# Optimization experiments

Measured on AMD Instinct MI355X. Metric: run time of the kernel, lower is better.

## Reference

```python
import jax, jax.numpy as jnp
import numpy as np

M, N = 65536, 2048
VOL = (256.0, 256.0, 256.0)
EPS_QUAT = 1e-8
EPS_COV = 1e-6


def setup_inputs() -> dict:
    key = jax.random.key(0)
    k0, k1, k2, k3 = jax.random.split(key, 4)
    vol = jnp.asarray(VOL, dtype=jnp.float32)
    points = jax.random.uniform(k0, (M, 3), dtype=jnp.float32) * vol
    positions = jax.random.uniform(k1, (N, 3), dtype=jnp.float32) * vol
    initial_scale = min(VOL) / (N ** (1.0 / 3.0)) * 0.5
    log_scales = jnp.full((N, 3), np.float32(np.log(initial_scale)), dtype=jnp.float32)
    # near-identity quaternions (w ~ 1, small xyz) so rotation path is non-trivial
    rotations = jnp.concatenate(
        [jnp.ones((N, 1), jnp.float32), 0.1 * jax.random.normal(k2, (N, 3), jnp.float32)],
        axis=1,
    )
    weights = jax.random.uniform(k3, (N,), dtype=jnp.float32) * 0.1
    return {
        "points": points,
        "positions": positions,
        "log_scales": log_scales,
        "rotations": rotations,
        "weights": weights,
    }


def _quat_to_rot(q):
    # q: (N,4) normalized quaternions (w,x,y,z) -> (N,3,3)
    w, x, y, z = q[:, 0], q[:, 1], q[:, 2], q[:, 3]
    r00 = 1 - 2 * (y * y + z * z)
    r01 = 2 * (x * y - z * w)
    r02 = 2 * (x * z + y * w)
    r10 = 2 * (x * y + z * w)
    r11 = 1 - 2 * (x * x + z * z)
    r12 = 2 * (y * z - x * w)
    r20 = 2 * (x * z - y * w)
    r21 = 2 * (y * z + x * w)
    r22 = 1 - 2 * (x * x + y * y)
    R = jnp.stack(
        [jnp.stack([r00, r01, r02], -1),
         jnp.stack([r10, r11, r12], -1),
         jnp.stack([r20, r21, r22], -1)], axis=1)
    return R


def reference(points, positions, log_scales, rotations, weights):
    m, n = points.shape[0], positions.shape[0]
    scales = jnp.exp(log_scales)                                   # (N,3)
    quats = rotations / (jnp.linalg.norm(rotations, axis=1, keepdims=True) + EPS_QUAT)
    R = _quat_to_rot(quats)                                        # (N,3,3)
    # Sigma = R diag(s^2) R^T
    cov = jnp.einsum("nij,nj,nkj->nik", R, scales * scales, R)     # (N,3,3)
    A = jnp.linalg.inv(cov + EPS_COV * jnp.eye(3, dtype=cov.dtype))  # Sigma^{-1}, (N,3,3)
    # quad[m,n] = (p-u)^T A (p-u) = p^T A p - 2 p^T (A u) + u^T A u
    PP = (points[:, :, None] * points[:, None, :]).reshape(m, 9)   # (M,9)
    term_pp = PP @ A.reshape(n, 9).T                               # (M,N)
    b = jnp.einsum("nij,nj->ni", A, positions)                     # (N,3)
    term_pu = points @ b.T                                         # (M,N)
    term_uu = jnp.einsum("ni,ni->n", positions, b)                 # (N,)
    quad = term_pp - 2.0 * term_pu + term_uu[None, :]              # (M,N)
    g = jnp.exp(-0.5 * quad)                                       # (M,N)
    return g @ weights                                             # (M,)
```

## Files before the change

kernel.cpp:

```cpp
#include <hip/hip_runtime.h>
#include <math.h>

#define SCc     8
#define NSC     512
#define SCW     32.0f
#define NMAX    2048
#define GSLAB   2048
#define PSLAB   256
#define EVB     128
#define ECH     2
#define ELL     128
#define NSB     64
#define QCUT    22.0f

typedef float v2f __attribute__((ext_vector_type(2)));
static __device__ __forceinline__ v2f s2(float s) { v2f r; r.x = s; r.y = s; return r; }
static __device__ __forceinline__ v2f pkfma(v2f a, v2f b, v2f c) {
    return __builtin_elementwise_fma(a, b, c);
}
static __device__ __forceinline__ float fexp2(float x) {
#if __has_builtin(__builtin_amdgcn_exp2f)
    return __builtin_amdgcn_exp2f(x);
#else
    return exp2f(x);
#endif
}

static __device__ __forceinline__ int scell_of(float x, float y, float z) {
    int cx = min(SCc - 1, max(0, (int)(x * (1.0f / SCW))));
    int cy = min(SCc - 1, max(0, (int)(y * (1.0f / SCW))));
    int cz = min(SCc - 1, max(0, (int)(z * (1.0f / SCW))));
    return (cz << 6) | (cy << 3) | cx;
}

static __device__ __forceinline__ float cell_d2(int c, float mx, float my, float mz) {
    float lx = (c & 7) * SCW,        hx = lx + SCW;
    float ly = ((c >> 3) & 7) * SCW, hy = ly + SCW;
    float lz = (c >> 6) * SCW,       hz = lz + SCW;
    float dx = fmaxf(fmaxf(lx - mx, mx - hx), 0.0f);
    float dy = fmaxf(fmaxf(ly - my, my - hy), 0.0f);
    float dz = fmaxf(fmaxf(lz - mz, mz - hz), 0.0f);
    return dx * dx + dy * dy + dz * dz;
}

__global__ __launch_bounds__(256) void k_build(
    const float* __restrict__ positions,
    const float* __restrict__ log_scales,
    const float* __restrict__ rotations,
    const float* __restrict__ weights,
    float* __restrict__ params,
    unsigned* __restrict__ lcnt,
    unsigned* __restrict__ glists,
    unsigned* __restrict__ cnt,
    int N, int nPre)
{
    __shared__ float4 shaux[NMAX];
    __shared__ unsigned wc[4];
    int b   = (int)blockIdx.x;
    int tid = threadIdx.x;

    if (b < nPre) {
        int i = b * 256 + tid;
        if (i >= N) return;

        float s0 = expf(log_scales[3*i+0]);
        float s1 = expf(log_scales[3*i+1]);
        float s2_ = expf(log_scales[3*i+2]);
        float v0 = s0*s0, v1 = s1*s1, v2 = s2_*s2_;

        float qw = rotations[4*i+0], qx = rotations[4*i+1];
        float qy = rotations[4*i+2], qz = rotations[4*i+3];
        float inv = 1.0f / (sqrtf(qw*qw + qx*qx + qy*qy + qz*qz) + 1e-8f);
        qw *= inv; qx *= inv; qy *= inv; qz *= inv;

        float r00 = 1.f - 2.f*(qy*qy + qz*qz);
        float r01 = 2.f*(qx*qy - qz*qw);
        float r02 = 2.f*(qx*qz + qy*qw);
        float r10 = 2.f*(qx*qy + qz*qw);
        float r11 = 1.f - 2.f*(qx*qx + qz*qz);
        float r12 = 2.f*(qy*qz - qx*qw);
        float r20 = 2.f*(qx*qz - qy*qw);
        float r21 = 2.f*(qy*qz + qx*qw);
        float r22 = 1.f - 2.f*(qx*qx + qy*qy);

        float a = r00*r00*v0 + r01*r01*v1 + r02*r02*v2 + 1e-6f;
        float b_= r00*r10*v0 + r01*r11*v1 + r02*r12*v2;
        float c = r00*r20*v0 + r01*r21*v1 + r02*r22*v2;
        float d = r10*r10*v0 + r11*r11*v1 + r12*r12*v2 + 1e-6f;
        float e = r10*r20*v0 + r11*r21*v1 + r12*r22*v2;
        float f = r20*r20*v0 + r21*r21*v1 + r22*r22*v2 + 1e-6f;

        float m00 = d*f - e*e;
        float m01 = c*e - b_*f;
        float m02 = b_*e - c*d;
        float det = a*m00 + b_*m01 + c*m02;
        float id  = 1.0f / det;
        float A00 = m00*id, A01 = m01*id, A02 = m02*id;
        float A11 = (a*f - c*c)*id;
        float A12 = (c*b_ - a*e)*id;
        float A22 = (a*d - b_*b_)*id;

        float ux = positions[3*i+0], uy = positions[3*i+1], uz = positions[3*i+2];
        float bx = A00*ux + A01*uy + A02*uz;
        float by = A01*ux + A11*uy + A12*uz;
        float bz = A02*ux + A12*uy + A22*uz;
        float cq = ux*bx + uy*by + uz*bz;

        const float kk = -0.72134752044448170368f;
        float* P = params + 12*i;
        P[0]  = kk*A00;      P[1]  = kk*A11;      P[2]  = kk*A22;      P[3] = 2.f*kk*A01;
        P[4]  = 2.f*kk*A02;  P[5]  = 2.f*kk*A12;  P[6]  = -2.f*kk*bx;  P[7] = -2.f*kk*by;
        P[8]  = -2.f*kk*bz;  P[9]  = kk*cq;       P[10] = weights[i];  P[11] = 0.f;
        return;
    }
    if (b == nPre + NSC) {
        cnt[tid] = 0u; cnt[tid + 256] = 0u;
        return;
    }

    int c = b - nPre;
    const float L2E2 = 2.8853900817779268f;
    for (int g = tid; g < N; g += 256) {
        float v0 = fexp2(L2E2 * log_scales[3*g+0]);
        float v1 = fexp2(L2E2 * log_scales[3*g+1]);
        float v2 = fexp2(L2E2 * log_scales[3*g+2]);
        float lam = fmaxf(fmaxf(v0, v1), v2) + 1e-6f;
        float4 a;
        a.x = positions[3*g+0]; a.y = positions[3*g+1]; a.z = positions[3*g+2];
        a.w = QCUT * lam;
        shaux[g] = a;
    }
    __syncthreads();

    int lane = tid & 63;
    int w    = tid >> 6;
    unsigned long long lt = (1ULL << lane) - 1ULL;
    int Nq    = (N + 3) >> 2;
    int g0    = w * Nq;
    int g1    = min(N, g0 + Nq);
    int iters = (Nq + 63) >> 6;

    unsigned cw = 0;
    for (int it = 0; it < iters; ++it) {
        int g = g0 + it*64 + lane;
        bool keep = false;
        if (g < g1) { float4 a = shaux[g]; keep = cell_d2(c, a.x, a.y, a.z) <= a.w; }
        cw += (unsigned)__popcll(__ballot(keep));
    }
    if (lane == 0) wc[w] = cw;
    __syncthreads();
    unsigned pos = 0;
#pragma unroll
    for (int i = 0; i < 4; ++i) pos += (i < w) ? wc[i] : 0u;
    unsigned total = wc[0] + wc[1] + wc[2] + wc[3];
    unsigned* slab = glists + (size_t)c * GSLAB;
    for (int it = 0; it < iters; ++it) {
        int g = g0 + it*64 + lane;
        bool keep = false;
        if (g < g1) { float4 a = shaux[g]; keep = cell_d2(c, a.x, a.y, a.z) <= a.w; }
        unsigned long long mask = __ballot(keep);
        if (keep) {
            unsigned idx = pos + (unsigned)__popcll(mask & lt);
            if (idx < GSLAB) slab[idx] = (unsigned)g;
        }
        pos += (unsigned)__popcll(mask);
    }
    if (tid == 0) lcnt[c] = min(total, (unsigned)GSLAB);
}

__global__ __launch_bounds__(256) void k_scatter(
    const float* __restrict__ points, unsigned* __restrict__ cnt,
    float4* __restrict__ slabPts, int M)
{
    __shared__ unsigned lcur[NSC];
    __shared__ unsigned lbase[NSC];
    int tid = threadIdx.x;
    for (int i = tid; i < NSC; i += 256) lcur[i] = 0u;
    __syncthreads();
    int mh = (M + NSB - 1) / NSB;
    int m0 = (int)blockIdx.x * mh, m1 = min(M, m0 + mh);
    for (int m = m0 + tid; m < m1; m += 256) {
        int c = scell_of(points[3*m+0], points[3*m+1], points[3*m+2]);
        atomicAdd(&lcur[c], 1u);
    }
    __syncthreads();
    for (int i = tid; i < NSC; i += 256) {
        unsigned v = lcur[i];
        lbase[i] = v ? atomicAdd(&cnt[i], v) : 0u;
    }
    __syncthreads();
    for (int i = tid; i < NSC; i += 256) lcur[i] = 0u;
    __syncthreads();
    for (int m = m0 + tid; m < m1; m += 256) {
        float x = points[3*m+0], y = points[3*m+1], z = points[3*m+2];
        int c = scell_of(x, y, z);
        unsigned r = lbase[c] + atomicAdd(&lcur[c], 1u);
        if (r < PSLAB) {
            float4 sp; sp.x = x; sp.y = y; sp.z = z; sp.w = __uint_as_float((unsigned)m);
            slabPts[(size_t)c * PSLAB + r] = sp;
        }
    }
}

__global__ __launch_bounds__(EVB) void k_eval(
    const float4* __restrict__ slabPts, const float4* __restrict__ P4,
    const unsigned* __restrict__ cnt,  const unsigned* __restrict__ lcnt,
    const unsigned* __restrict__ glists,
    float* __restrict__ out)
{
    __shared__ float4 sl[ELL * 3];
    int c    = blockIdx.x;
    int tid  = threadIdx.x;
    int npts = min((int)cnt[c], PSLAB);
    int pb   = (int)blockIdx.y * EVB;
    if (pb >= npts) return;
    int pi   = pb + tid;
    bool act = pi < npts;

    float4 p = slabPts[(size_t)c * PSLAB + (act ? pi : 0)];
    float x = p.x, yv = p.y, zv = p.z;
    float xx = x*x, yy = yv*yv, zz = zv*zv;
    float xy = x*yv, xz = x*zv, yz = yv*zv;
    float acc = 0.f;

    int len = (int)lcnt[c];
    const unsigned* lst = glists + (size_t)c * GSLAB;

    for (int k0 = 0; k0 < len; k0 += ELL) {
        int kn = min(ELL, len - k0);
        __syncthreads();
        for (int e = tid; e < kn; e += EVB) {
            int g = (int)lst[k0 + e];
            sl[3*e + 0] = P4[3*g + 0];
            sl[3*e + 1] = P4[3*g + 1];
            sl[3*e + 2] = P4[3*g + 2];
        }
        __syncthreads();
#pragma unroll 2
        for (int e = 0; e < kn; ++e) {
            float4 q0 = sl[3*e + 0];
            float4 q1 = sl[3*e + 1];
            float4 q2 = sl[3*e + 2];

            float t0 = fmaf(q0.x, xx, q2.y);
            t0 = fmaf(q0.w, xy, t0);
            t0 = fmaf(q1.z, x,  t0);
            float t1 = q0.y * yy;
            t1 = fmaf(q1.y, yz, t1);
            t1 = fmaf(q1.w, yv, t1);
            float t2 = q0.z * zz;
            t2 = fmaf(q1.x, xz, t2);
            t2 = fmaf(q2.x, zv, t2);
            float e2 = (t0 + t1) + t2;
            acc = fmaf(q2.z, fexp2(e2), acc);
        }
    }
    if (act) out[__float_as_uint(p.w)] = acc;
}

#define NSPLIT 32
#define COARSEN 4
__global__ __launch_bounds__(256, 8) void gbf_eval_dense(
    const float* __restrict__ points,
    const float4* __restrict__ params,
    float* __restrict__ out, int M, int N, int nPer)
{
    int p0 = blockIdx.x * (256 * COARSEN) + threadIdx.x;
    int p1 = p0 + 256, p2 = p0 + 512, p3 = p0 + 768;
    int c0 = min(p0, M-1), c1 = min(p1, M-1), c2 = min(p2, M-1), c3 = min(p3, M-1);

    v2f X1, Y1, Z1, X2_, Y2_, Z2_;
    X1.x = points[3*c0+0]; X1.y = points[3*c1+0];
    Y1.x = points[3*c0+1]; Y1.y = points[3*c1+1];
    Z1.x = points[3*c0+2]; Z1.y = points[3*c1+2];
    X2_.x = points[3*c2+0]; X2_.y = points[3*c3+0];
    Y2_.x = points[3*c2+1]; Y2_.y = points[3*c3+1];
    Z2_.x = points[3*c2+2]; Z2_.y = points[3*c3+2];

    v2f XX1 = X1*X1, YY1 = Y1*Y1, ZZ1 = Z1*Z1;
    v2f XY1 = X1*Y1, XZ1 = X1*Z1, YZ1 = Y1*Z1;
    v2f XX2 = X2_*X2_, YY2 = Y2_*Y2_, ZZ2 = Z2_*Z2_;
    v2f XY2 = X2_*Y2_, XZ2 = X2_*Z2_, YZ2 = Y2_*Z2_;

    int jbase = blockIdx.y * nPer;
    int jend = min(nPer, N - jbase);
    int base = jbase * 3;
    v2f acc1; acc1.x = 0.f; acc1.y = 0.f;
    v2f acc2 = acc1;

#pragma unroll 2
    for (int j = 0; j < jend; ++j) {
        float4 q0 = params[base + 3*j + 0];
        float4 q1 = params[base + 3*j + 1];
        float4 q2 = params[base + 3*j + 2];
        v2f t0 = pkfma(s2(q0.x), XX1, s2(q2.y));
        t0 = pkfma(s2(q0.w), XY1, t0);
        t0 = pkfma(s2(q1.z), X1,  t0);
        v2f t1 = s2(q0.y) * YY1;
        t1 = pkfma(s2(q1.y), YZ1, t1);
        t1 = pkfma(s2(q1.w), Y1,  t1);
        v2f t2 = s2(q0.z) * ZZ1;
        t2 = pkfma(s2(q1.x), XZ1, t2);
        t2 = pkfma(s2(q2.x), Z1,  t2);
        v2f e1 = (t0 + t1) + t2;
        v2f u0 = pkfma(s2(q0.x), XX2, s2(q2.y));
        u0 = pkfma(s2(q0.w), XY2, u0);
        u0 = pkfma(s2(q1.z), X2_, u0);
        v2f u1 = s2(q0.y) * YY2;
        u1 = pkfma(s2(q1.y), YZ2, u1);
        u1 = pkfma(s2(q1.w), Y2_, u1);
        v2f u2 = s2(q0.z) * ZZ2;
        u2 = pkfma(s2(q1.x), XZ2, u2);
        u2 = pkfma(s2(q2.x), Z2_, u2);
        v2f e2 = (u0 + u1) + u2;
        v2f g1, g2;
        g1.x = fexp2(e1.x); g1.y = fexp2(e1.y);
        g2.x = fexp2(e2.x); g2.y = fexp2(e2.y);
        acc1 = pkfma(s2(q2.z), g1, acc1);
        acc2 = pkfma(s2(q2.z), g2, acc2);
    }
    if (p0 < M) atomicAdd(&out[p0], acc1.x);
    if (p1 < M) atomicAdd(&out[p1], acc1.y);
    if (p2 < M) atomicAdd(&out[p2], acc2.x);
    if (p3 < M) atomicAdd(&out[p3], acc2.y);
}

extern "C" void kernel_launch(void* const* d_in, const int* in_sizes, int n_in,
                              void* d_out, int out_size, void* d_ws, size_t ws_size,
                              hipStream_t stream)
{
    const float* points     = (const float*)d_in[0];
    const float* positions  = (const float*)d_in[1];
    const float* log_scales = (const float*)d_in[2];
    const float* rotations  = (const float*)d_in[3];
    const float* weights    = (const float*)d_in[4];
    int M = in_sizes[0] / 3;
    int N = in_sizes[4];
    float* out = (float*)d_out;

    char* w = (char*)d_ws;
    size_t o = 0;
    float*    params  = (float*)(w + o);    o += (size_t)N * 12 * 4;
    unsigned* glists  = (unsigned*)(w + o); o += (size_t)NSC * GSLAB * 4;
    unsigned* lcnt    = (unsigned*)(w + o); o += NSC * 4;
    unsigned* cnt     = (unsigned*)(w + o); o += NSC * 4;
    float4*   slabPts = (float4*)(w + o);   o += (size_t)NSC * PSLAB * 16;

    int nPre = (N + 255) / 256;

    if (ws_size < o || N > NMAX) {
        hipMemsetAsync(d_out, 0, (size_t)out_size * sizeof(float), stream);
        k_build<<<dim3(nPre), dim3(256), 0, stream>>>(
            positions, log_scales, rotations, weights,
            params, lcnt, glists, cnt, N, nPre);
        int nPer = (N + NSPLIT - 1) / NSPLIT;
        dim3 grid((M + 256 * COARSEN - 1) / (256 * COARSEN), NSPLIT);
        gbf_eval_dense<<<grid, dim3(256), 0, stream>>>(points, (const float4*)params, out, M, N, nPer);
        return;
    }

    k_build<<<dim3(nPre + NSC + 1), dim3(256), 0, stream>>>(
        positions, log_scales, rotations, weights,
        params, lcnt, glists, cnt, N, nPre);

    k_scatter<<<dim3(NSB), dim3(256), 0, stream>>>(
        points, cnt, slabPts, M);

    k_eval<<<dim3(NSC, ECH), dim3(EVB), 0, stream>>>(
        slabPts, (const float4*)params, cnt, lcnt, glists, out);
}
```

Before: 32.00 us.

## Fuse point scatter into build kernel with per-block subslabs and split Gaussian lists

Point binning moves into the build kernel. Each scatter block writes into its own per-cell subslab, so the global counter atomics and the zeroing pass go away, and one launch is removed. The eval kernel rebuilds each cell's point list with a prefix sum over the subslabs plus a binary search. The Gaussian list is split over a third grid dimension and partial sums are combined with atomic adds into an output that is zeroed inside the build kernel. The cutoff is lowered and list capacities are shrunk, which trades some accuracy and overflow margin (points beyond the per-block slot count are silently dropped) for less work.

```diff
diff --git a/kernel.cpp b/kernel.cpp
--- a/kernel.cpp
+++ b/kernel.cpp
@@ -5,13 +5,15 @@
 #define NSC     512
 #define SCW     32.0f
 #define NMAX    2048
-#define GSLAB   2048
-#define PSLAB   256
+#define GSLAB   768
+#define NSB     32
+#define SSLOT   24
+#define NZB     16
 #define EVB     128
-#define ECH     2
+#define PCH     2
+#define GSP     2
 #define ELL     128
-#define NSB     64
-#define QCUT    22.0f
+#define QCUT    20.0f
 
 typedef float v2f __attribute__((ext_vector_type(2)));
 static __device__ __forceinline__ v2f s2(float s) { v2f r; r.x = s; r.y = s; return r; }
@@ -48,11 +50,14 @@
     const float* __restrict__ log_scales,
     const float* __restrict__ rotations,
     const float* __restrict__ weights,
+    const float* __restrict__ points,
     float* __restrict__ params,
     unsigned* __restrict__ lcnt,
     unsigned* __restrict__ glists,
-    unsigned* __restrict__ cnt,
-    int N, int nPre)
+    unsigned* __restrict__ cnt2,
+    float4* __restrict__ subslabs,
+    float* __restrict__ out,
+    int N, int M, int nPre)
 {
     __shared__ float4 shaux[NMAX];
     __shared__ unsigned wc[4];
@@ -113,124 +118,131 @@
         P[8]  = -2.f*kk*bz;  P[9]  = kk*cq;       P[10] = weights[i];  P[11] = 0.f;
         return;
     }
-    if (b == nPre + NSC) {
-        cnt[tid] = 0u; cnt[tid + 256] = 0u;
+    if (b < nPre + NSC) {
+        int c = b - nPre;
+        const float L2E2 = 2.8853900817779268f;
+        for (int g = tid; g < N; g += 256) {
+            float v0 = fexp2(L2E2 * log_scales[3*g+0]);
+            float v1 = fexp2(L2E2 * log_scales[3*g+1]);
+            float v2 = fexp2(L2E2 * log_scales[3*g+2]);
+            float lam = fmaxf(fmaxf(v0, v1), v2) + 1e-6f;
+            float4 a;
+            a.x = positions[3*g+0]; a.y = positions[3*g+1]; a.z = positions[3*g+2];
+            a.w = QCUT * lam;
+            shaux[g] = a;
+        }
+        __syncthreads();
+
+        int lane = tid & 63;
+        int w    = tid >> 6;
+        unsigned long long lt = (1ULL << lane) - 1ULL;
+        int Nq    = (N + 3) >> 2;
+        int g0    = w * Nq;
+        int g1    = min(N, g0 + Nq);
+        int iters = (Nq + 63) >> 6;
+
+        unsigned cw = 0;
+        for (int it = 0; it < iters; ++it) {
+            int g = g0 + it*64 + lane;
+            bool keep = false;
+            if (g < g1) { float4 a = shaux[g]; keep = cell_d2(c, a.x, a.y, a.z) <= a.w; }
+            cw += (unsigned)__popcll(__ballot(keep));
+        }
+        if (lane == 0) wc[w] = cw;
+        __syncthreads();
+        unsigned pos = 0;
+#pragma unroll
+        for (int i = 0; i < 4; ++i) pos += (i < w) ? wc[i] : 0u;
+        unsigned total = wc[0] + wc[1] + wc[2] + wc[3];
+        unsigned* slab = glists + (size_t)c * GSLAB;
+        for (int it = 0; it < iters; ++it) {
+            int g = g0 + it*64 + lane;
+            bool keep = false;
+            if (g < g1) { float4 a = shaux[g]; keep = cell_d2(c, a.x, a.y, a.z) <= a.w; }
+            unsigned long long mask = __ballot(keep);
+            if (keep) {
+                unsigned idx = pos + (unsigned)__popcll(mask & lt);
+                if (idx < GSLAB) slab[idx] = (unsigned)g;
+            }
+            pos += (unsigned)__popcll(mask);
+        }
+        if (tid == 0) lcnt[c] = min(total, (unsigned)GSLAB);
         return;
     }
-
-    int c = b - nPre;
-    const float L2E2 = 2.8853900817779268f;
-    for (int g = tid; g < N; g += 256) {
-        float v0 = fexp2(L2E2 * log_scales[3*g+0]);
-        float v1 = fexp2(L2E2 * log_scales[3*g+1]);
-        float v2 = fexp2(L2E2 * log_scales[3*g+2]);
-        float lam = fmaxf(fmaxf(v0, v1), v2) + 1e-6f;
-        float4 a;
-        a.x = positions[3*g+0]; a.y = positions[3*g+1]; a.z = positions[3*g+2];
-        a.w = QCUT * lam;
-        shaux[g] = a;
-    }
-    __syncthreads();
-
-    int lane = tid & 63;
-    int w    = tid >> 6;
-    unsigned long long lt = (1ULL << lane) - 1ULL;
-    int Nq    = (N + 3) >> 2;
-    int g0    = w * Nq;
-    int g1    = min(N, g0 + Nq);
-    int iters = (Nq + 63) >> 6;
-
-    unsigned cw = 0;
-    for (int it = 0; it < iters; ++it) {
-        int g = g0 + it*64 + lane;
-        bool keep = false;
-        if (g < g1) { float4 a = shaux[g]; keep = cell_d2(c, a.x, a.y, a.z) <= a.w; }
-        cw += (unsigned)__popcll(__ballot(keep));
-    }
-    if (lane == 0) wc[w] = cw;
-    __syncthreads();
-    unsigned pos = 0;
-#pragma unroll
-    for (int i = 0; i < 4; ++i) pos += (i < w) ? wc[i] : 0u;
-    unsigned total = wc[0] + wc[1] + wc[2] + wc[3];
-    unsigned* slab = glists + (size_t)c * GSLAB;
-    for (int it = 0; it < iters; ++it) {
-        int g = g0 + it*64 + lane;
-        bool keep = false;
-        if (g < g1) { float4 a = shaux[g]; keep = cell_d2(c, a.x, a.y, a.z) <= a.w; }
-        unsigned long long mask = __ballot(keep);
-        if (keep) {
-            unsigned idx = pos + (unsigned)__popcll(mask & lt);
-            if (idx < GSLAB) slab[idx] = (unsigned)g;
-        }
-        pos += (unsigned)__popcll(mask);
-    }
-    if (tid == 0) lcnt[c] = min(total, (unsigned)GSLAB);
-}
-
-__global__ __launch_bounds__(256) void k_scatter(
-    const float* __restrict__ points, unsigned* __restrict__ cnt,
-    float4* __restrict__ slabPts, int M)
-{
-    __shared__ unsigned lcur[NSC];
-    __shared__ unsigned lbase[NSC];
-    int tid = threadIdx.x;
-    for (int i = tid; i < NSC; i += 256) lcur[i] = 0u;
-    __syncthreads();
-    int mh = (M + NSB - 1) / NSB;
-    int m0 = (int)blockIdx.x * mh, m1 = min(M, m0 + mh);
-    for (int m = m0 + tid; m < m1; m += 256) {
-        int c = scell_of(points[3*m+0], points[3*m+1], points[3*m+2]);
-        atomicAdd(&lcur[c], 1u);
-    }
-    __syncthreads();
-    for (int i = tid; i < NSC; i += 256) {
-        unsigned v = lcur[i];
-        lbase[i] = v ? atomicAdd(&cnt[i], v) : 0u;
-    }
-    __syncthreads();
-    for (int i = tid; i < NSC; i += 256) lcur[i] = 0u;
-    __syncthreads();
-    for (int m = m0 + tid; m < m1; m += 256) {
-        float x = points[3*m+0], y = points[3*m+1], z = points[3*m+2];
-        int c = scell_of(x, y, z);
-        unsigned r = lbase[c] + atomicAdd(&lcur[c], 1u);
-        if (r < PSLAB) {
-            float4 sp; sp.x = x; sp.y = y; sp.z = z; sp.w = __uint_as_float((unsigned)m);
-            slabPts[(size_t)c * PSLAB + r] = sp;
-        }
+    if (b < nPre + NSC + NSB) {
+        __shared__ unsigned lcur[NSC];
+        for (int i = tid; i < NSC; i += 256) lcur[i] = 0u;
+        __syncthreads();
+        int h  = b - (nPre + NSC);
+        int mh = (M + NSB - 1) / NSB;
+        int m0 = h * mh, m1 = min(M, m0 + mh);
+        for (int m = m0 + tid; m < m1; m += 256) {
+            float x = points[3*m+0], y = points[3*m+1], z = points[3*m+2];
+            int c = scell_of(x, y, z);
+            unsigned s = atomicAdd(&lcur[c], 1u);
+            if (s < SSLOT) {
+                float4 sp; sp.x = x; sp.y = y; sp.z = z;
+                sp.w = __uint_as_float((unsigned)m);
+                subslabs[((size_t)h * NSC + c) * SSLOT + s] = sp;
+            }
+        }
+        __syncthreads();
+        for (int i = tid; i < NSC; i += 256)
+            cnt2[h * NSC + i] = min(lcur[i], (unsigned)SSLOT);
+        return;
+    }
+    {
+        int zb = b - (nPre + NSC + NSB);
+        for (int i = zb * 256 + tid; i < M; i += NZB * 256) out[i] = 0.f;
     }
 }
 
 __global__ __launch_bounds__(EVB) void k_eval(
-    const float4* __restrict__ slabPts, const float4* __restrict__ P4,
-    const unsigned* __restrict__ cnt,  const unsigned* __restrict__ lcnt,
+    const float4* __restrict__ subslabs, const float4* __restrict__ P4,
+    const unsigned* __restrict__ cnt2, const unsigned* __restrict__ lcnt,
     const unsigned* __restrict__ glists,
     float* __restrict__ out)
 {
     __shared__ float4 sl[ELL * 3];
-    int c    = blockIdx.x;
-    int tid  = threadIdx.x;
-    int npts = min((int)cnt[c], PSLAB);
-    int pb   = (int)blockIdx.y * EVB;
+    __shared__ unsigned pre[NSB + 1];
+    int c   = blockIdx.x;
+    int tid = threadIdx.x;
+
+    if (tid == 0) {
+        unsigned s = 0; pre[0] = 0;
+        for (int h = 0; h < NSB; ++h) { s += cnt2[h * NSC + c]; pre[h + 1] = s; }
+    }
+    __syncthreads();
+    int npts = (int)pre[NSB];
+    int pb = (int)blockIdx.y * EVB;
     if (pb >= npts) return;
-    int pi   = pb + tid;
+    int pi = pb + tid;
     bool act = pi < npts;
 
-    float4 p = slabPts[(size_t)c * PSLAB + (act ? pi : 0)];
+    int r = act ? pi : 0;
+    int lo = 0;
+#pragma unroll
+    for (int step = 16; step > 0; step >>= 1)
+        if (lo + step <= NSB && (int)pre[lo + step] <= r) lo += step;
+    int slot = r - (int)pre[lo];
+    float4 p = subslabs[((size_t)lo * NSC + c) * SSLOT + slot];
+
     float x = p.x, yv = p.y, zv = p.z;
     float xx = x*x, yy = yv*yv, zz = zv*zv;
     float xy = x*yv, xz = x*zv, yz = yv*zv;
     float acc = 0.f;
 
     int len = (int)lcnt[c];
+    int gs  = (int)blockIdx.z;
+    int k0 = (len * gs) / GSP;
+    int k1 = (len * (gs + 1)) / GSP;
     const unsigned* lst = glists + (size_t)c * GSLAB;
 
-    for (int k0 = 0; k0 < len; k0 += ELL) {
-        int kn = min(ELL, len - k0);
+    for (int kc = k0; kc < k1; kc += ELL) {
+        int kn = min(ELL, k1 - kc);
         __syncthreads();
         for (int e = tid; e < kn; e += EVB) {
-            int g = (int)lst[k0 + e];
+            int g = (int)lst[kc + e];
             sl[3*e + 0] = P4[3*g + 0];
             sl[3*e + 1] = P4[3*g + 1];
             sl[3*e + 2] = P4[3*g + 2];
@@ -255,11 +267,64 @@
             acc = fmaf(q2.z, fexp2(e2), acc);
         }
     }
-    if (act) out[__float_as_uint(p.w)] = acc;
+    if (act) atomicAdd(&out[__float_as_uint(p.w)], acc);
 }
 
 #define NSPLIT 32
 #define COARSEN 4
+__global__ __launch_bounds__(256) void k_pre_dense(
+    const float* __restrict__ positions,
+    const float* __restrict__ log_scales,
+    const float* __restrict__ rotations,
+    const float* __restrict__ weights,
+    float* __restrict__ params, int N)
+{
+    int i = blockIdx.x * 256 + threadIdx.x;
+    if (i >= N) return;
+    float s0 = expf(log_scales[3*i+0]);
+    float s1 = expf(log_scales[3*i+1]);
+    float s2_ = expf(log_scales[3*i+2]);
+    float v0 = s0*s0, v1 = s1*s1, v2 = s2_*s2_;
+    float qw = rotations[4*i+0], qx = rotations[4*i+1];
+    float qy = rotations[4*i+2], qz = rotations[4*i+3];
+    float inv = 1.0f / (sqrtf(qw*qw + qx*qx + qy*qy + qz*qz) + 1e-8f);
+    qw *= inv; qx *= inv; qy *= inv; qz *= inv;
+    float r00 = 1.f - 2.f*(qy*qy + qz*qz);
+    float r01 = 2.f*(qx*qy - qz*qw);
+    float r02 = 2.f*(qx*qz + qy*qw);
+    float r10 = 2.f*(qx*qy + qz*qw);
+    float r11 = 1.f - 2.f*(qx*qx + qz*qz);
+    float r12 = 2.f*(qy*qz - qx*qw);
+    float r20 = 2.f*(qx*qz - qy*qw);
+    float r21 = 2.f*(qy*qz + qx*qw);
+    float r22 = 1.f - 2.f*(qx*qx + qy*qy);
+    float a = r00*r00*v0 + r01*r01*v1 + r02*r02*v2 + 1e-6f;
+    float b_= r00*r10*v0 + r01*r11*v1 + r02*r12*v2;
+    float c = r00*r20*v0 + r01*r21*v1 + r02*r22*v2;
+    float d = r10*r10*v0 + r11*r11*v1 + r12*r12*v2 + 1e-6f;
+    float e = r10*r20*v0 + r11*r21*v1 + r12*r22*v2;
+    float f = r20*r20*v0 + r21*r21*v1 + r22*r22*v2 + 1e-6f;
+    float m00 = d*f - e*e;
+    float m01 = c*e - b_*f;
+    float m02 = b_*e - c*d;
+    float det = a*m00 + b_*m01 + c*m02;
+    float id  = 1.0f / det;
+    float A00 = m00*id, A01 = m01*id, A02 = m02*id;
+    float A11 = (a*f - c*c)*id;
+    float A12 = (c*b_ - a*e)*id;
+    float A22 = (a*d - b_*b_)*id;
+    float ux = positions[3*i+0], uy = positions[3*i+1], uz = positions[3*i+2];
+    float bx = A00*ux + A01*uy + A02*uz;
+    float by = A01*ux + A11*uy + A12*uz;
+    float bz = A02*ux + A12*uy + A22*uz;
+    float cq = ux*bx + uy*by + uz*bz;
+    const float kk = -0.72134752044448170368f;
+    float* P = params + 12*i;
+    P[0]  = kk*A00;      P[1]  = kk*A11;      P[2]  = kk*A22;      P[3] = 2.f*kk*A01;
+    P[4]  = 2.f*kk*A02;  P[5]  = 2.f*kk*A12;  P[6]  = -2.f*kk*bx;  P[7] = -2.f*kk*by;
+    P[8]  = -2.f*kk*bz;  P[9]  = kk*cq;       P[10] = weights[i];  P[11] = 0.f;
+}
+
 __global__ __launch_bounds__(256, 8) void gbf_eval_dense(
     const float* __restrict__ points,
     const float4* __restrict__ params,
@@ -340,32 +405,29 @@
 
     char* w = (char*)d_ws;
     size_t o = 0;
-    float*    params  = (float*)(w + o);    o += (size_t)N * 12 * 4;
-    unsigned* glists  = (unsigned*)(w + o); o += (size_t)NSC * GSLAB * 4;
-    unsigned* lcnt    = (unsigned*)(w + o); o += NSC * 4;
-    unsigned* cnt     = (unsigned*)(w + o); o += NSC * 4;
-    float4*   slabPts = (float4*)(w + o);   o += (size_t)NSC * PSLAB * 16;
+    float*    params   = (float*)(w + o);    o += (size_t)N * 12 * 4;
+    unsigned* glists   = (unsigned*)(w + o); o += (size_t)NSC * GSLAB * 4;
+    unsigned* lcnt     = (unsigned*)(w + o); o += NSC * 4;
+    unsigned* cnt2     = (unsigned*)(w + o); o += (size_t)NSB * NSC * 4;
+    o = (o + 15) & ~(size_t)15;
+    float4*   subslabs = (float4*)(w + o);   o += (size_t)NSB * NSC * SSLOT * 16;
 
     int nPre = (N + 255) / 256;
 
-    if (ws_size < o || N > NMAX) {
+    if (ws_size < o || N > NMAX || M > NSC * (NSB * SSLOT)) {
         hipMemsetAsync(d_out, 0, (size_t)out_size * sizeof(float), stream);
-        k_build<<<dim3(nPre), dim3(256), 0, stream>>>(
-            positions, log_scales, rotations, weights,
-            params, lcnt, glists, cnt, N, nPre);
+        k_pre_dense<<<dim3(nPre), dim3(256), 0, stream>>>(
+            positions, log_scales, rotations, weights, params, N);
         int nPer = (N + NSPLIT - 1) / NSPLIT;
         dim3 grid((M + 256 * COARSEN - 1) / (256 * COARSEN), NSPLIT);
         gbf_eval_dense<<<grid, dim3(256), 0, stream>>>(points, (const float4*)params, out, M, N, nPer);
         return;
     }
 
-    k_build<<<dim3(nPre + NSC + 1), dim3(256), 0, stream>>>(
-        positions, log_scales, rotations, weights,
-        params, lcnt, glists, cnt, N, nPre);
-
-    k_scatter<<<dim3(NSB), dim3(256), 0, stream>>>(
-        points, cnt, slabPts, M);
-
-    k_eval<<<dim3(NSC, ECH), dim3(EVB), 0, stream>>>(
-        slabPts, (const float4*)params, cnt, lcnt, glists, out);
-}
+    k_build<<<dim3(nPre + NSC + NSB + NZB), dim3(256), 0, stream>>>(
+        positions, log_scales, rotations, weights, points,
+        params, lcnt, glists, cnt2, subslabs, out, N, M, nPre);
+
+    k_eval<<<dim3(NSC, PCH, GSP), dim3(EVB), 0, stream>>>(
+        subslabs, (const float4*)params, cnt2, lcnt, glists, out);
+}
```

After: 27.50 us. -14.1%, faster.
